# Kernel tuning notes

Measured on AMD Instinct MI355X. Metric: run time of the kernel, lower is better.

The kernel has to match this reference:

```python
import jax, jax.numpy as jnp
import numpy as np

EPS = 1e-8

def l2norm(x, axis=-1):
    norm = jnp.sqrt(jnp.sum(x * x, axis=axis, keepdims=True)) + EPS
    return x / norm

def setup_inputs() -> dict:
    key = jax.random.key(0)
    ks = jax.random.split(key, 4)
    B, Lq, Ls, d, sim_dim = 128, 128, 256, 1024, 256
    query = jax.random.normal(ks[0], (B, Lq, d), dtype=jnp.float32)
    context = jax.random.normal(ks[1], (B, Ls, d), dtype=jnp.float32)
    matrix = jax.random.uniform(ks[2], (B, Lq, d), dtype=jnp.float32)
    W = jax.random.normal(ks[3], (sim_dim, d), dtype=jnp.float32) * (1.0 / np.sqrt(d))
    b = jnp.zeros((sim_dim,), dtype=jnp.float32)
    smooth = 9
    return {"query": query, "context": context, "matrix": matrix, "W": W, "b": b, "smooth": smooth}

def reference(query, context, matrix, W, b, smooth):
    # cross_attention
    q = query * matrix                                   # (B, Lq, d)
    attn = jnp.einsum('bsd,bqd->bsq', context, q)        # (B, Ls, Lq)
    attn = jnp.where(attn >= 0, attn, 0.1 * attn)        # LeakyReLU(0.1)
    attn = l2norm(attn, axis=-1)                         # normalize over Lq
    attn = jnp.swapaxes(attn, 1, 2)                      # (B, Lq, Ls)
    attn = jax.nn.softmax(attn * smooth, axis=2)         # softmax over source
    wcontext = jnp.einsum('bqs,bsd->bqd', attn, context) # (B, Lq, d)
    wcontext = l2norm(wcontext, axis=-1)
    # alignment vector
    sim_rep = (query - wcontext) ** 2                    # (B, Lq, d)
    sim_rep = jnp.einsum('bqd,kd->bqk', sim_rep, W) + b  # Linear d -> sim_dim
    sim_rep = l2norm(sim_rep, axis=-1)
    return sim_rep
```

## Files before the change

kernel.cpp:

```cpp
#include <hip/hip_runtime.h>
#include <hip/hip_bf16.h>

constexpr int B  = 128;
constexpr int LQ = 128;
constexpr int LS = 256;
constexpr int D  = 1024;
constexpr int SD = 256;
constexpr float EPS = 1e-8f;

typedef __attribute__((ext_vector_type(8))) __bf16 bf16x8;
typedef __attribute__((ext_vector_type(4))) float f32x4;

__device__ inline ushort f2bf(float f) {
    union { float f; uint u; } v{f};
    uint r = v.u + 0x7fffu + ((v.u >> 16) & 1u);
    return (ushort)(r >> 16);
}
__device__ inline float bf2f(ushort u) {
    union { uint u; float f; } v{(uint)u << 16};
    return v.f;
}
__device__ inline uint4 pack8(float4 a, float4 b) {
    union { ushort us[8]; uint4 u4; } r;
    r.us[0]=f2bf(a.x); r.us[1]=f2bf(a.y); r.us[2]=f2bf(a.z); r.us[3]=f2bf(a.w);
    r.us[4]=f2bf(b.x); r.us[5]=f2bf(b.y); r.us[6]=f2bf(b.z); r.us[7]=f2bf(b.w);
    return r.u4;
}
__device__ inline int swz(int row, int kbyte) {
    return row * 128 + (kbyte ^ ((row & 7) << 4));
}
__device__ inline bf16x8 lds_frag(const ushort* base, int row, int kk, int lane) {
    int kbyte = kk * 64 + (lane >> 4) * 16;
    return *(const bf16x8*)((const char*)base + swz(row, kbyte));
}
__device__ inline int swz512(int row, int kbyte) {
    return row * 512 + (kbyte ^ ((row & 7) << 4));
}
__device__ inline f32x4 mfma16(bf16x8 a, bf16x8 b, f32x4 c) {
    return __builtin_amdgcn_mfma_f32_16x16x32_bf16(a, b, c, 0, 0, 0);
}

__global__ __launch_bounds__(256) void wconv_kernel(
    const float* __restrict__ W, ushort* __restrict__ Wb)
{
    size_t i = ((size_t)blockIdx.x * 256 + threadIdx.x) * 8;
    float4 a = *(const float4*)(W + i);
    float4 b = *(const float4*)(W + i + 4);
    *(uint4*)(Wb + i) = pack8(a, b);
}

__global__ __launch_bounds__(512) void gemmA_kernel(
    const float* __restrict__ query, const float* __restrict__ mat,
    const float* __restrict__ ctx, const int* __restrict__ smooth_p,
    ushort* __restrict__ E, ushort* __restrict__ ctxT)
{
    const int bid = blockIdx.x;
    const int xcd = bid & 7, idx = bid >> 3;
    const int b  = xcd * 16 + (idx >> 2);
    const int n0 = (idx & 3) * 64;
    __shared__ ushort As[2][128 * 64];
    __shared__ ushort Bs[2][64 * 64];
    __shared__ float colssP[2][64];
    __shared__ float invsm[64];
    const int t = threadIdx.x;
    const int wv = t >> 6, l = t & 63;
    const int wq = wv >> 2, wsv = wv & 3;

    const float* Qb = query + (size_t)b * LQ * D;
    const float* Mb = mat   + (size_t)b * LQ * D;
    const float* Cb = ctx   + ((size_t)b * LS + n0) * D;
    const int r0 = t >> 3, k8 = (t & 7) * 8;

    const int ed = t >> 3;
    const int es = (t & 7) * 8;
    ushort* CTb = ctxT + (size_t)b * D * LS + n0 + es;

    f32x4 acc[4] = {};
    float4 q0, q1, q2, q3, m0, m1, m2, m3, c0, c1;

    {
        const float* qp = Qb + (size_t)r0 * D + k8;
        const float* mp = Mb + (size_t)r0 * D + k8;
        q0 = *(const float4*)qp;  q1 = *(const float4*)(qp + 4);
        m0 = *(const float4*)mp;  m1 = *(const float4*)(mp + 4);
        qp += (size_t)64 * D;  mp += (size_t)64 * D;
        q2 = *(const float4*)qp;  q3 = *(const float4*)(qp + 4);
        m2 = *(const float4*)mp;  m3 = *(const float4*)(mp + 4);
        const float* cp = Cb + (size_t)r0 * D + k8;
        c0 = *(const float4*)cp;  c1 = *(const float4*)(cp + 4);
    }
    {
        float4 p1{q0.x*m0.x, q0.y*m0.y, q0.z*m0.z, q0.w*m0.w};
        float4 p2{q1.x*m1.x, q1.y*m1.y, q1.z*m1.z, q1.w*m1.w};
        *(uint4*)((char*)As[0] + swz(r0, k8 * 2)) = pack8(p1, p2);
        float4 p3{q2.x*m2.x, q2.y*m2.y, q2.z*m2.z, q2.w*m2.w};
        float4 p4{q3.x*m3.x, q3.y*m3.y, q3.z*m3.z, q3.w*m3.w};
        *(uint4*)((char*)As[0] + swz(r0 + 64, k8 * 2)) = pack8(p3, p4);
        *(uint4*)((char*)Bs[0] + swz(r0, k8 * 2)) = pack8(c0, c1);
    }
    __syncthreads();

    int cur = 0;
#pragma unroll 1
    for (int ks = 0; ks < 15; ++ks) {
        const int k0 = (ks + 1) * 64;
        {
            const float* qp = Qb + (size_t)r0 * D + k0 + k8;
            const float* mp = Mb + (size_t)r0 * D + k0 + k8;
            q0 = *(const float4*)qp;  q1 = *(const float4*)(qp + 4);
            m0 = *(const float4*)mp;  m1 = *(const float4*)(mp + 4);
            qp += (size_t)64 * D;  mp += (size_t)64 * D;
            q2 = *(const float4*)qp;  q3 = *(const float4*)(qp + 4);
            m2 = *(const float4*)mp;  m3 = *(const float4*)(mp + 4);
            const float* cp = Cb + (size_t)r0 * D + k0 + k8;
            c0 = *(const float4*)cp;  c1 = *(const float4*)(cp + 4);
        }
#pragma unroll
        for (int kk = 0; kk < 2; ++kk) {
            bf16x8 bfr = lds_frag(Bs[cur], wsv * 16 + (l & 15), kk, l);
#pragma unroll
            for (int i = 0; i < 4; ++i) {
                bf16x8 af = lds_frag(As[cur], wq * 64 + i * 16 + (l & 15), kk, l);
                acc[i] = mfma16(af, bfr, acc[i]);
            }
        }
        {
            uint4 tv;
            ushort* tp = (ushort*)&tv;
#pragma unroll
            for (int j = 0; j < 8; ++j)
                tp[j] = *(const ushort*)((const char*)Bs[cur] + swz(es + j, ed * 2));
            *(uint4*)(CTb + (size_t)(ks * 64 + ed) * LS) = tv;
        }
        {
            float4 p1{q0.x*m0.x, q0.y*m0.y, q0.z*m0.z, q0.w*m0.w};
            float4 p2{q1.x*m1.x, q1.y*m1.y, q1.z*m1.z, q1.w*m1.w};
            *(uint4*)((char*)As[cur ^ 1] + swz(r0, k8 * 2)) = pack8(p1, p2);
            float4 p3{q2.x*m2.x, q2.y*m2.y, q2.z*m2.z, q2.w*m2.w};
            float4 p4{q3.x*m3.x, q3.y*m3.y, q3.z*m3.z, q3.w*m3.w};
            *(uint4*)((char*)As[cur ^ 1] + swz(r0 + 64, k8 * 2)) = pack8(p3, p4);
            *(uint4*)((char*)Bs[cur ^ 1] + swz(r0, k8 * 2)) = pack8(c0, c1);
        }
        __syncthreads();
        cur ^= 1;
    }
#pragma unroll
    for (int kk = 0; kk < 2; ++kk) {
        bf16x8 bfr = lds_frag(Bs[cur], wsv * 16 + (l & 15), kk, l);
#pragma unroll
        for (int i = 0; i < 4; ++i) {
            bf16x8 af = lds_frag(As[cur], wq * 64 + i * 16 + (l & 15), kk, l);
            acc[i] = mfma16(af, bfr, acc[i]);
        }
    }
    {
        uint4 tv;
        ushort* tp = (ushort*)&tv;
#pragma unroll
        for (int j = 0; j < 8; ++j)
            tp[j] = *(const ushort*)((const char*)Bs[cur] + swz(es + j, ed * 2));
        *(uint4*)(CTb + (size_t)(15 * 64 + ed) * LS) = tv;
    }

    float csum = 0.f;
#pragma unroll
    for (int i = 0; i < 4; ++i)
#pragma unroll
        for (int r = 0; r < 4; ++r) {
            float v = acc[i][r];
            v = v >= 0.f ? v : 0.1f * v;
            acc[i][r] = v;
            csum += v * v;
        }
    csum += __shfl_xor(csum, 16);
    csum += __shfl_xor(csum, 32);
    if (l < 16) colssP[wq][wsv * 16 + l] = csum;
    __syncthreads();
    const float sm = (float)(*smooth_p);
    if (t < 64) invsm[t] = sm / (sqrtf(colssP[0][t] + colssP[1][t]) + EPS);
    __syncthreads();
    const float invc = invsm[wsv * 16 + (l & 15)];
    ushort* Eb = E + (size_t)b * LQ * LS + n0 + wsv * 16 + (l & 15);
#pragma unroll
    for (int i = 0; i < 4; ++i)
#pragma unroll
        for (int r = 0; r < 4; ++r) {
            int row = wq * 64 + i * 16 + (l >> 4) * 4 + r;
            Eb[(size_t)row * LS] = f2bf(__expf(acc[i][r] * invc));
        }
}

__global__ __launch_bounds__(512) void pv_kernel(
    const ushort* __restrict__ E, const ushort* __restrict__ ctxT,
    ushort* __restrict__ wctx, float* __restrict__ rowssP)
{
    const int bid = blockIdx.x;
    const int xcd = bid & 7, idx = bid >> 3;
    const int b  = xcd * 16 + (idx >> 2);
    const int qh = (idx >> 1) & 1, dh = idx & 1;
    __shared__ ushort Es[64 * 256];
    __shared__ ushort Bs[64 * 256];
    __shared__ float rsumL[64];
    __shared__ float rinv[64];
    __shared__ float rowssL[64][4];
    const int t = threadIdx.x;
    const int wv = t >> 6, l = t & 63;
    const int wq = wv >> 2, wd = wv & 3;
    const int cc = t & 31, rr = t >> 5;

    const ushort* Eb = E + ((size_t)b * LQ + qh * 64) * LS;
    float part[4];
#pragma unroll
    for (int it = 0; it < 4; ++it) {
        int row = rr + it * 16;
        uint4 v = *(const uint4*)(Eb + (size_t)row * LS + cc * 8);
        *(uint4*)((char*)Es + swz512(row, cc * 16)) = v;
        const ushort* us = (const ushort*)&v;
        float s = 0.f;
#pragma unroll
        for (int j = 0; j < 8; ++j) s += bf2f(us[j]);
        part[it] = s;
    }
    if (t < 256) rowssL[t >> 2][t & 3] = 0.f;
#pragma unroll
    for (int it = 0; it < 4; ++it) {
        float s = part[it];
        s += __shfl_xor(s, 1);  s += __shfl_xor(s, 2);
        s += __shfl_xor(s, 4);  s += __shfl_xor(s, 8);
        s += __shfl_xor(s, 16);
        if ((l & 31) == 0) rsumL[rr + it * 16] = s;
    }
    __syncthreads();
    if (t < 64) rinv[t] = 1.0f / rsumL[t];
    __syncthreads();

    bf16x8 af[2][8];
#pragma unroll
    for (int i = 0; i < 2; ++i)
#pragma unroll
        for (int kk = 0; kk < 8; ++kk)
            af[i][kk] = *(const bf16x8*)((const char*)Es +
                swz512(wq * 32 + i * 16 + (l & 15), kk * 64 + (l >> 4) * 16));

    const ushort* Cb = ctxT + ((size_t)b * D + dh * 512) * LS;
    ushort* Ob = wctx + ((size_t)b * LQ + qh * 64) * D + dh * 512;

#pragma unroll 1
    for (int dt = 0; dt < 8; ++dt) {
        __syncthreads();
#pragma unroll
        for (int it = 0; it < 4; ++it) {
            int row = rr + it * 16;
            uint4 v = *(const uint4*)(Cb + (size_t)(dt * 64 + row) * LS + cc * 8);
            *(uint4*)((char*)Bs + swz512(row, cc * 16)) = v;
        }
        __syncthreads();
        f32x4 acc[2] = {};
#pragma unroll
        for (int kk = 0; kk < 8; ++kk) {
            bf16x8 bfr = *(const bf16x8*)((const char*)Bs +
                swz512(wd * 16 + (l & 15), kk * 64 + (l >> 4) * 16));
            acc[0] = mfma16(af[0][kk], bfr, acc[0]);
            acc[1] = mfma16(af[1][kk], bfr, acc[1]);
        }
#pragma unroll
        for (int i = 0; i < 2; ++i)
#pragma unroll
            for (int r = 0; r < 4; ++r) {
                int row = wq * 32 + i * 16 + (l >> 4) * 4 + r;
                float wval = acc[i][r] * rinv[row];
                float p2 = wval * wval;
                p2 += __shfl_xor(p2, 1); p2 += __shfl_xor(p2, 2);
                p2 += __shfl_xor(p2, 4); p2 += __shfl_xor(p2, 8);
                if ((l & 15) == 0) rowssL[row][wd] += p2;
                Ob[(size_t)row * D + dt * 64 + wd * 16 + (l & 15)] = f2bf(wval);
            }
    }
    __syncthreads();
    if (t < 64)
        rowssP[(size_t)b * 256 + dh * 128 + qh * 64 + t] =
            rowssL[t][0] + rowssL[t][1] + rowssL[t][2] + rowssL[t][3];
}

__global__ __launch_bounds__(512) void gemm3_kernel(
    const ushort* __restrict__ wctx, const float* __restrict__ query,
    const float* __restrict__ rowssP, const ushort* __restrict__ Wb,
    const float* __restrict__ bias, float* __restrict__ out)
{
    const int m0 = blockIdx.x * 64;
    const int b  = blockIdx.y;
    __shared__ ushort As[64 * 64];
    __shared__ ushort Bs[256 * 64];
    __shared__ float red[64][4];
    __shared__ float invr[64];
    const int t = threadIdx.x;
    const int w = t >> 6, l = t & 63;
    const int wm = (w >> 2) * 32, wn = (w & 3) * 64;

    const int arow = t >> 3, ako = (t & 7) * 8;
    const float r0v = rowssP[(size_t)b * 256 + m0 + arow];
    const float r1v = rowssP[(size_t)b * 256 + 128 + m0 + arow];
    const float ivq = 1.0f / (sqrtf(r0v + r1v) + EPS);
    const float* Qp  = query + ((size_t)b * LQ + m0 + arow) * D + ako;
    const ushort* Wp = wctx  + ((size_t)b * LQ + m0 + arow) * D + ako;

    f32x4 acc[2][4] = {};

    for (int k0 = 0; k0 < D; k0 += 64) {
        if (k0) __syncthreads();
        {
            uint4 wu = *(const uint4*)(Wp + k0);
            float4 q1 = *(const float4*)(Qp + k0);
            float4 q2 = *(const float4*)(Qp + k0 + 4);
            float d0 = q1.x - bf2f((ushort)(wu.x & 0xffff)) * ivq;
            float d1 = q1.y - bf2f((ushort)(wu.x >> 16))    * ivq;
            float d2 = q1.z - bf2f((ushort)(wu.y & 0xffff)) * ivq;
            float d3 = q1.w - bf2f((ushort)(wu.y >> 16))    * ivq;
            float d4 = q2.x - bf2f((ushort)(wu.z & 0xffff)) * ivq;
            float d5 = q2.y - bf2f((ushort)(wu.z >> 16))    * ivq;
            float d6 = q2.z - bf2f((ushort)(wu.w & 0xffff)) * ivq;
            float d7 = q2.w - bf2f((ushort)(wu.w >> 16))    * ivq;
            float4 s1{d0*d0, d1*d1, d2*d2, d3*d3};
            float4 s2{d4*d4, d5*d5, d6*d6, d7*d7};
            *(uint4*)((char*)As + swz(arow, ako * 2)) = pack8(s1, s2);
        }
#pragma unroll
        for (int j = 0; j < 4; ++j) {
            int c = t + j * 512;
            int row = c >> 3, ko = (c & 7) * 8;
            *(uint4*)((char*)Bs + swz(row, ko * 2)) =
                *(const uint4*)(Wb + (size_t)row * D + k0 + ko);
        }
        __syncthreads();
#pragma unroll
        for (int kk = 0; kk < 2; ++kk) {
            bf16x8 af[2], bfr[4];
#pragma unroll
            for (int i = 0; i < 2; ++i) af[i] = lds_frag(As, wm + i * 16 + (l & 15), kk, l);
#pragma unroll
            for (int n = 0; n < 4; ++n) bfr[n] = lds_frag(Bs, wn + n * 16 + (l & 15), kk, l);
#pragma unroll
            for (int i = 0; i < 2; ++i)
#pragma unroll
                for (int n = 0; n < 4; ++n) acc[i][n] = mfma16(af[i], bfr[n], acc[i][n]);
        }
    }
#pragma unroll
    for (int n = 0; n < 4; ++n) {
        float bv = bias[wn + n * 16 + (l & 15)];
#pragma unroll
        for (int i = 0; i < 2; ++i)
#pragma unroll
            for (int r = 0; r < 4; ++r) acc[i][n][r] += bv;
    }
#pragma unroll
    for (int i = 0; i < 2; ++i)
#pragma unroll
        for (int r = 0; r < 4; ++r) {
            float p = 0.f;
#pragma unroll
            for (int n = 0; n < 4; ++n) p += acc[i][n][r] * acc[i][n][r];
#pragma unroll
            for (int off = 1; off < 16; off <<= 1) p += __shfl_xor(p, off);
            int rowl = wm + i * 16 + (l >> 4) * 4 + r;
            if ((l & 15) == 0) red[rowl][w & 3] = p;
        }
    __syncthreads();
    if (t < 64) {
        float s = red[t][0] + red[t][1] + red[t][2] + red[t][3];
        invr[t] = 1.0f / (sqrtf(s) + EPS);
    }
    __syncthreads();
    float* Ob = out + ((size_t)b * LQ + m0) * SD;
#pragma unroll
    for (int i = 0; i < 2; ++i)
#pragma unroll
        for (int r = 0; r < 4; ++r) {
            int rowl = wm + i * 16 + (l >> 4) * 4 + r;
            float iv = invr[rowl];
#pragma unroll
            for (int n = 0; n < 4; ++n) {
                int col = wn + n * 16 + (l & 15);
                Ob[(size_t)rowl * SD + col] = acc[i][n][r] * iv;
            }
        }
}

extern "C" void kernel_launch(void* const* d_in, const int* in_sizes, int n_in,
                              void* d_out, int out_size, void* d_ws, size_t ws_size,
                              hipStream_t stream)
{
    const float* query  = (const float*)d_in[0];
    const float* ctx    = (const float*)d_in[1];
    const float* mat    = (const float*)d_in[2];
    const float* W      = (const float*)d_in[3];
    const float* bias   = (const float*)d_in[4];
    const int*   smooth = (const int*)d_in[5];
    float* out = (float*)d_out;

    char* ws = (char*)d_ws;
    ushort* ctxT   = (ushort*)ws;
    ushort* wctx   = (ushort*)(ws + (size_t)64 * 1024 * 1024);
    ushort* E      = (ushort*)(ws + (size_t)96 * 1024 * 1024);
    ushort* Wb     = (ushort*)(ws + (size_t)104 * 1024 * 1024);
    float*  rowssP = (float*)(ws + (size_t)(104 * 1024 + 512) * 1024);

    wconv_kernel<<<dim3(SD * D / (256 * 8)), 256, 0, stream>>>(W, Wb);
    gemmA_kernel<<<dim3(512), 512, 0, stream>>>(query, mat, ctx, smooth, E, ctxT);
    pv_kernel<<<dim3(512), 512, 0, stream>>>(E, ctxT, wctx, rowssP);
    gemm3_kernel<<<dim3(2, B), 512, 0, stream>>>(wctx, query, rowssP, Wb, bias, out);
}
```

Before: 162.8 us.

## Drop ctxT intermediate; PV kernel reads fp32 context directly and transposes in LDS

gemmA no longer writes a transposed bf16 copy of context to global memory. Instead pv_kernel loads fp32 context tiles itself, converts them to bf16 and transposes them into a padded LDS buffer, prefetching the next tile in registers. pv_kernel now covers all 128 query rows per block with half as many blocks, so each context tile is loaded once per batch/d-half rather than twice. This removes a 64MB write and a 64MB read, but adds fp32 reads of context, scalar LDS transpose stores and lower occupancy from the larger LDS footprint.

```diff
diff --git a/kernel.cpp b/kernel.cpp
--- a/kernel.cpp
+++ b/kernel.cpp
@@ -52,7 +52,7 @@
 __global__ __launch_bounds__(512) void gemmA_kernel(
     const float* __restrict__ query, const float* __restrict__ mat,
     const float* __restrict__ ctx, const int* __restrict__ smooth_p,
-    ushort* __restrict__ E, ushort* __restrict__ ctxT)
+    ushort* __restrict__ E)
 {
     const int bid = blockIdx.x;
     const int xcd = bid & 7, idx = bid >> 3;
@@ -70,10 +70,6 @@
     const float* Mb = mat   + (size_t)b * LQ * D;
     const float* Cb = ctx   + ((size_t)b * LS + n0) * D;
     const int r0 = t >> 3, k8 = (t & 7) * 8;
-
-    const int ed = t >> 3;
-    const int es = (t & 7) * 8;
-    ushort* CTb = ctxT + (size_t)b * D * LS + n0 + es;
 
     f32x4 acc[4] = {};
     float4 q0, q1, q2, q3, m0, m1, m2, m3, c0, c1;
@@ -125,14 +121,6 @@
             }
         }
         {
-            uint4 tv;
-            ushort* tp = (ushort*)&tv;
-#pragma unroll
-            for (int j = 0; j < 8; ++j)
-                tp[j] = *(const ushort*)((const char*)Bs[cur] + swz(es + j, ed * 2));
-            *(uint4*)(CTb + (size_t)(ks * 64 + ed) * LS) = tv;
-        }
-        {
             float4 p1{q0.x*m0.x, q0.y*m0.y, q0.z*m0.z, q0.w*m0.w};
             float4 p2{q1.x*m1.x, q1.y*m1.y, q1.z*m1.z, q1.w*m1.w};
             *(uint4*)((char*)As[cur ^ 1] + swz(r0, k8 * 2)) = pack8(p1, p2);
@@ -153,14 +141,6 @@
             acc[i] = mfma16(af, bfr, acc[i]);
         }
     }
-    {
-        uint4 tv;
-        ushort* tp = (ushort*)&tv;
-#pragma unroll
-        for (int j = 0; j < 8; ++j)
-            tp[j] = *(const ushort*)((const char*)Bs[cur] + swz(es + j, ed * 2));
-        *(uint4*)(CTb + (size_t)(15 * 64 + ed) * LS) = tv;
-    }
 
     float csum = 0.f;
 #pragma unroll
@@ -191,83 +171,95 @@
 }
 
 __global__ __launch_bounds__(512) void pv_kernel(
-    const ushort* __restrict__ E, const ushort* __restrict__ ctxT,
+    const ushort* __restrict__ E, const float* __restrict__ ctx,
     ushort* __restrict__ wctx, float* __restrict__ rowssP)
 {
     const int bid = blockIdx.x;
     const int xcd = bid & 7, idx = bid >> 3;
-    const int b  = xcd * 16 + (idx >> 2);
-    const int qh = (idx >> 1) & 1, dh = idx & 1;
-    __shared__ ushort Es[64 * 256];
-    __shared__ ushort Bs[64 * 256];
-    __shared__ float rsumL[64];
-    __shared__ float rinv[64];
-    __shared__ float rowssL[64][4];
+    const int b  = xcd * 16 + (idx >> 1);
+    const int dh = idx & 1;
+    const int dglob0 = dh * 512;
+
+    __shared__ ushort Es[128 * 256];
+    __shared__ ushort Bs[64 * 264];
+    __shared__ float rsumL[128];
+    __shared__ float rinv[128];
+    __shared__ float rowssL[128][4];
+
     const int t = threadIdx.x;
     const int wv = t >> 6, l = t & 63;
     const int wq = wv >> 2, wd = wv & 3;
+
+    const ushort* Eb = E + (size_t)b * LQ * LS;
     const int cc = t & 31, rr = t >> 5;
-
-    const ushort* Eb = E + ((size_t)b * LQ + qh * 64) * LS;
-    float part[4];
-#pragma unroll
-    for (int it = 0; it < 4; ++it) {
-        int row = rr + it * 16;
+    float part[8];
+#pragma unroll
+    for (int p = 0; p < 8; ++p) {
+        int row = rr + p * 16;
         uint4 v = *(const uint4*)(Eb + (size_t)row * LS + cc * 8);
         *(uint4*)((char*)Es + swz512(row, cc * 16)) = v;
         const ushort* us = (const ushort*)&v;
         float s = 0.f;
 #pragma unroll
         for (int j = 0; j < 8; ++j) s += bf2f(us[j]);
-        part[it] = s;
-    }
-    if (t < 256) rowssL[t >> 2][t & 3] = 0.f;
-#pragma unroll
-    for (int it = 0; it < 4; ++it) {
-        float s = part[it];
+        part[p] = s;
+    }
+    rowssL[t >> 2][t & 3] = 0.f;
+#pragma unroll
+    for (int p = 0; p < 8; ++p) {
+        float s = part[p];
         s += __shfl_xor(s, 1);  s += __shfl_xor(s, 2);
         s += __shfl_xor(s, 4);  s += __shfl_xor(s, 8);
         s += __shfl_xor(s, 16);
-        if ((l & 31) == 0) rsumL[rr + it * 16] = s;
-    }
-    __syncthreads();
-    if (t < 64) rinv[t] = 1.0f / rsumL[t];
-    __syncthreads();
-
-    bf16x8 af[2][8];
-#pragma unroll
-    for (int i = 0; i < 2; ++i)
-#pragma unroll
-        for (int kk = 0; kk < 8; ++kk)
-            af[i][kk] = *(const bf16x8*)((const char*)Es +
-                swz512(wq * 32 + i * 16 + (l & 15), kk * 64 + (l >> 4) * 16));
-
-    const ushort* Cb = ctxT + ((size_t)b * D + dh * 512) * LS;
-    ushort* Ob = wctx + ((size_t)b * LQ + qh * 64) * D + dh * 512;
+        if ((l & 31) == 0) rsumL[rr + p * 16] = s;
+    }
+
+    const float* Cb = ctx + (size_t)b * LS * D + dglob0;
+    const int sr = t >> 4, c4 = (t & 15) * 4;
+    float4 cr[8];
+#pragma unroll
+    for (int p = 0; p < 8; ++p)
+        cr[p] = *(const float4*)(Cb + (size_t)(p * 32 + sr) * D + c4);
+
+    __syncthreads();
+    if (t < 128) rinv[t] = 1.0f / rsumL[t];
+
+#pragma unroll
+    for (int p = 0; p < 8; ++p) {
+        int s = p * 32 + sr;
+        Bs[(c4 + 0) * 264 + s] = f2bf(cr[p].x);
+        Bs[(c4 + 1) * 264 + s] = f2bf(cr[p].y);
+        Bs[(c4 + 2) * 264 + s] = f2bf(cr[p].z);
+        Bs[(c4 + 3) * 264 + s] = f2bf(cr[p].w);
+    }
+    __syncthreads();
+
+    ushort* Ob = wctx + (size_t)b * LQ * D + dglob0;
 
 #pragma unroll 1
     for (int dt = 0; dt < 8; ++dt) {
-        __syncthreads();
-#pragma unroll
-        for (int it = 0; it < 4; ++it) {
-            int row = rr + it * 16;
-            uint4 v = *(const uint4*)(Cb + (size_t)(dt * 64 + row) * LS + cc * 8);
-            *(uint4*)((char*)Bs + swz512(row, cc * 16)) = v;
-        }
-        __syncthreads();
-        f32x4 acc[2] = {};
+        if (dt < 7) {
+#pragma unroll
+            for (int p = 0; p < 8; ++p)
+                cr[p] = *(const float4*)(Cb + (size_t)(p * 32 + sr) * D + (dt + 1) * 64 + c4);
+        }
+        f32x4 acc[4] = {};
 #pragma unroll
         for (int kk = 0; kk < 8; ++kk) {
-            bf16x8 bfr = *(const bf16x8*)((const char*)Bs +
-                swz512(wd * 16 + (l & 15), kk * 64 + (l >> 4) * 16));
-            acc[0] = mfma16(af[0][kk], bfr, acc[0]);
-            acc[1] = mfma16(af[1][kk], bfr, acc[1]);
-        }
-#pragma unroll
-        for (int i = 0; i < 2; ++i)
+            const ushort* bp = Bs + (wd * 16 + (l & 15)) * 264 + kk * 32 + (l >> 4) * 8;
+            bf16x8 bfr = *(const bf16x8*)bp;
+#pragma unroll
+            for (int i = 0; i < 4; ++i) {
+                bf16x8 af = *(const bf16x8*)((const char*)Es +
+                    swz512(wq * 64 + i * 16 + (l & 15), kk * 64 + (l >> 4) * 16));
+                acc[i] = mfma16(af, bfr, acc[i]);
+            }
+        }
+#pragma unroll
+        for (int i = 0; i < 4; ++i)
 #pragma unroll
             for (int r = 0; r < 4; ++r) {
-                int row = wq * 32 + i * 16 + (l >> 4) * 4 + r;
+                int row = wq * 64 + i * 16 + (l >> 4) * 4 + r;
                 float wval = acc[i][r] * rinv[row];
                 float p2 = wval * wval;
                 p2 += __shfl_xor(p2, 1); p2 += __shfl_xor(p2, 2);
@@ -275,10 +267,21 @@
                 if ((l & 15) == 0) rowssL[row][wd] += p2;
                 Ob[(size_t)row * D + dt * 64 + wd * 16 + (l & 15)] = f2bf(wval);
             }
-    }
-    __syncthreads();
-    if (t < 64)
-        rowssP[(size_t)b * 256 + dh * 128 + qh * 64 + t] =
+        __syncthreads();
+        if (dt < 7) {
+#pragma unroll
+            for (int p = 0; p < 8; ++p) {
+                int s = p * 32 + sr;
+                Bs[(c4 + 0) * 264 + s] = f2bf(cr[p].x);
+                Bs[(c4 + 1) * 264 + s] = f2bf(cr[p].y);
+                Bs[(c4 + 2) * 264 + s] = f2bf(cr[p].z);
+                Bs[(c4 + 3) * 264 + s] = f2bf(cr[p].w);
+            }
+            __syncthreads();
+        }
+    }
+    if (t < 128)
+        rowssP[(size_t)b * 256 + dh * 128 + t] =
             rowssL[t][0] + rowssL[t][1] + rowssL[t][2] + rowssL[t][3];
 }
 
@@ -399,14 +402,13 @@
     float* out = (float*)d_out;
 
     char* ws = (char*)d_ws;
-    ushort* ctxT   = (ushort*)ws;
-    ushort* wctx   = (ushort*)(ws + (size_t)64 * 1024 * 1024);
-    ushort* E      = (ushort*)(ws + (size_t)96 * 1024 * 1024);
-    ushort* Wb     = (ushort*)(ws + (size_t)104 * 1024 * 1024);
-    float*  rowssP = (float*)(ws + (size_t)(104 * 1024 + 512) * 1024);
+    ushort* wctx   = (ushort*)ws;
+    ushort* E      = (ushort*)(ws + (size_t)32 * 1024 * 1024);
+    ushort* Wb     = (ushort*)(ws + (size_t)40 * 1024 * 1024);
+    float*  rowssP = (float*)(ws + (size_t)(40 * 1024 + 512) * 1024);
 
     wconv_kernel<<<dim3(SD * D / (256 * 8)), 256, 0, stream>>>(W, Wb);
-    gemmA_kernel<<<dim3(512), 512, 0, stream>>>(query, mat, ctx, smooth, E, ctxT);
-    pv_kernel<<<dim3(512), 512, 0, stream>>>(E, ctxT, wctx, rowssP);
+    gemmA_kernel<<<dim3(512), 512, 0, stream>>>(query, mat, ctx, smooth, E);
+    pv_kernel<<<dim3(256), 512, 0, stream>>>(E, ctx, wctx, rowssP);
     gemm3_kernel<<<dim3(2, B), 512, 0, stream>>>(wctx, query, rowssP, Wb, bias, out);
 }
```

New measurement: 156.3 us. -4.0%, faster.
